# Kernel optimization log

Hardware: AMD Instinct MI355X
Metric: run time of the kernel (lower is better)

## Reference

```python
import jax, jax.numpy as jnp
import numpy as np

CONF_THRES = 0.25  # init_kwargs: conf_thres
# output_type = 'all': loss accumulates class score (col 5) and box coord sum

N = 4_000_000

def setup_inputs() -> dict:
    key = jax.random.key(0)
    k1, k2 = jax.random.split(key)
    post_result = jax.random.uniform(k1, (N, 6), dtype=jnp.float32)
    pre_result_boxes = jax.random.normal(k2, (N, 4), dtype=jnp.float32)
    return {"post_result": post_result, "pre_result_boxes": pre_result_boxes}

def reference(post_result, pre_result_boxes):
    # mask of detections with confidence >= threshold
    mask = (post_result[:, 4] >= CONF_THRES).astype(post_result.dtype)  # [N]
    per_det = post_result[:, 5] + pre_result_boxes.sum(axis=-1)          # [N]
    loss = jnp.sum(mask * per_det)                                       # scalar
    # fallback: if loss is exactly 0.0, return post_result[..., 4].sum() * 0.0
    loss = jnp.where(loss == 0.0, post_result[:, 4].sum() * 0.0, loss)
    return loss
```

## Files before the change

### kernel.cpp

```cpp
#include <hip/hip_runtime.h>

#define CONF_THRES 0.25f

__device__ __forceinline__ float row_val(const float* __restrict__ post,
                                         const float* __restrict__ boxes, int i) {
    float2 cs = *reinterpret_cast<const float2*>(post + 6ll * i + 4);
    float4 b = *reinterpret_cast<const float4*>(boxes + 4ll * i);
    float per = cs.y + (b.x + b.y) + (b.z + b.w);
    return (cs.x >= CONF_THRES) ? per : 0.0f;
}

__global__ void __launch_bounds__(256) yolo_partial(const float* __restrict__ post,
                                                    const float* __restrict__ boxes,
                                                    float* __restrict__ partials, int n) {
    int tid = blockIdx.x * blockDim.x + threadIdx.x;
    int stride = gridDim.x * blockDim.x;

    float acc = 0.0f;
    int i = tid;
    for (; i + 3 * stride < n; i += 4 * stride) {
        float a0 = row_val(post, boxes, i);
        float a1 = row_val(post, boxes, i + stride);
        float a2 = row_val(post, boxes, i + 2 * stride);
        float a3 = row_val(post, boxes, i + 3 * stride);
        acc += (a0 + a1) + (a2 + a3);
    }
    for (; i < n; i += stride)
        acc += row_val(post, boxes, i);

    #pragma unroll
    for (int off = 32; off > 0; off >>= 1)
        acc += __shfl_down(acc, off, 64);

    __shared__ float ws[4];
    int wid = threadIdx.x >> 6;
    if ((threadIdx.x & 63) == 0) ws[wid] = acc;
    __syncthreads();
    if (threadIdx.x == 0)
        partials[blockIdx.x] = (ws[0] + ws[1]) + (ws[2] + ws[3]);
}

__global__ void __launch_bounds__(256) yolo_final(const float* __restrict__ partials,
                                                  float* __restrict__ out, int m) {
    float acc = 0.0f;
    for (int i = threadIdx.x; i < m; i += blockDim.x)
        acc += partials[i];

    #pragma unroll
    for (int off = 32; off > 0; off >>= 1)
        acc += __shfl_down(acc, off, 64);

    __shared__ float ws[4];
    int wid = threadIdx.x >> 6;
    if ((threadIdx.x & 63) == 0) ws[wid] = acc;
    __syncthreads();
    if (threadIdx.x == 0)
        out[0] = (ws[0] + ws[1]) + (ws[2] + ws[3]);
}

extern "C" void kernel_launch(void* const* d_in, const int* in_sizes, int n_in,
                              void* d_out, int out_size, void* d_ws, size_t ws_size,
                              hipStream_t stream) {
    const float* post  = (const float*)d_in[0];
    const float* boxes = (const float*)d_in[1];
    float* out = (float*)d_out;
    float* partials = (float*)d_ws;

    int n = in_sizes[0] / 6;

    const int block = 256;
    int blocks = 2048;
    int needed = (n + block - 1) / block;
    if (blocks > needed) blocks = needed;

    yolo_partial<<<blocks, block, 0, stream>>>(post, boxes, partials, n);
    yolo_final<<<1, block, 0, stream>>>(partials, out, blocks);
}
```

Measured before the change: 32.19 us.

## Fuse final reduction into partial kernel via last-block atomic counter

Merges the two-kernel reduction into one kernel: each block writes its partial, bumps an atomic counter, and the last block to finish sums all partials and writes the output. The main loop also changes from 4-way strided unrolling to a fixed 7-iteration unroll that covers the typical per-thread work, with a remainder loop. This removes a second kernel launch and its dependency gap, but adds a hipMemsetAsync to reset the counter, which may itself cost about as much as the launch it replaces.

```diff
diff --git a/kernel.cpp b/kernel.cpp
--- a/kernel.cpp
+++ b/kernel.cpp
@@ -10,52 +10,60 @@
     return (cs.x >= CONF_THRES) ? per : 0.0f;
 }
 
-__global__ void __launch_bounds__(256) yolo_partial(const float* __restrict__ post,
-                                                    const float* __restrict__ boxes,
-                                                    float* __restrict__ partials, int n) {
-    int tid = blockIdx.x * blockDim.x + threadIdx.x;
-    int stride = gridDim.x * blockDim.x;
+__global__ void __launch_bounds__(256) yolo_fused(const float* __restrict__ post,
+                                                  const float* __restrict__ boxes,
+                                                  float* __restrict__ partials,
+                                                  unsigned int* __restrict__ counter,
+                                                  float* __restrict__ out, int n) {
+    const int T = gridDim.x * blockDim.x;
+    const int tid = blockIdx.x * blockDim.x + threadIdx.x;
 
     float acc = 0.0f;
-    int i = tid;
-    for (; i + 3 * stride < n; i += 4 * stride) {
-        float a0 = row_val(post, boxes, i);
-        float a1 = row_val(post, boxes, i + stride);
-        float a2 = row_val(post, boxes, i + 2 * stride);
-        float a3 = row_val(post, boxes, i + 3 * stride);
-        acc += (a0 + a1) + (a2 + a3);
+    long i = tid;
+    if (7ll * T <= (long)n) {
+        #pragma unroll
+        for (int k = 0; k < 7; ++k) {
+            acc += row_val(post, boxes, (int)i);
+            i += T;
+        }
+        for (; i < n; i += T)
+            acc += row_val(post, boxes, (int)i);
+    } else {
+        for (; i < n; i += T)
+            acc += row_val(post, boxes, (int)i);
     }
-    for (; i < n; i += stride)
-        acc += row_val(post, boxes, i);
 
     #pragma unroll
     for (int off = 32; off > 0; off >>= 1)
         acc += __shfl_down(acc, off, 64);
 
     __shared__ float ws[4];
+    __shared__ bool is_last;
     int wid = threadIdx.x >> 6;
     if ((threadIdx.x & 63) == 0) ws[wid] = acc;
     __syncthreads();
-    if (threadIdx.x == 0)
+
+    if (threadIdx.x == 0) {
         partials[blockIdx.x] = (ws[0] + ws[1]) + (ws[2] + ws[3]);
-}
+        __threadfence();
+        unsigned old = atomicAdd(counter, 1u);
+        is_last = (old == gridDim.x - 1);
+    }
+    __syncthreads();
 
-__global__ void __launch_bounds__(256) yolo_final(const float* __restrict__ partials,
-                                                  float* __restrict__ out, int m) {
-    float acc = 0.0f;
-    for (int i = threadIdx.x; i < m; i += blockDim.x)
-        acc += partials[i];
-
-    #pragma unroll
-    for (int off = 32; off > 0; off >>= 1)
-        acc += __shfl_down(acc, off, 64);
-
-    __shared__ float ws[4];
-    int wid = threadIdx.x >> 6;
-    if ((threadIdx.x & 63) == 0) ws[wid] = acc;
-    __syncthreads();
-    if (threadIdx.x == 0)
-        out[0] = (ws[0] + ws[1]) + (ws[2] + ws[3]);
+    if (is_last) {
+        float a2 = 0.0f;
+        for (int j = threadIdx.x; j < (int)gridDim.x; j += blockDim.x)
+            a2 += __hip_atomic_load(&partials[j], __ATOMIC_RELAXED,
+                                    __HIP_MEMORY_SCOPE_AGENT);
+        #pragma unroll
+        for (int off = 32; off > 0; off >>= 1)
+            a2 += __shfl_down(a2, off, 64);
+        if ((threadIdx.x & 63) == 0) ws[wid] = a2;
+        __syncthreads();
+        if (threadIdx.x == 0)
+            out[0] = (ws[0] + ws[1]) + (ws[2] + ws[3]);
+    }
 }
 
 extern "C" void kernel_launch(void* const* d_in, const int* in_sizes, int n_in,
@@ -64,7 +72,9 @@
     const float* post  = (const float*)d_in[0];
     const float* boxes = (const float*)d_in[1];
     float* out = (float*)d_out;
-    float* partials = (float*)d_ws;
+
+    unsigned int* counter = (unsigned int*)d_ws;
+    float* partials = (float*)((char*)d_ws + 256);
 
     int n = in_sizes[0] / 6;
 
@@ -73,6 +83,7 @@
     int needed = (n + block - 1) / block;
     if (blocks > needed) blocks = needed;
 
-    yolo_partial<<<blocks, block, 0, stream>>>(post, boxes, partials, n);
-    yolo_final<<<1, block, 0, stream>>>(partials, out, blocks);
+    hipMemsetAsync(counter, 0, sizeof(unsigned int), stream);
+
+    yolo_fused<<<blocks, block, 0, stream>>>(post, boxes, partials, counter, out, n);
 }
```

Result: slower. 101.4 us (+214.9%).
